# Kernel tuning notes

Hardware: AMD Instinct MI355X
Metric: run time of the kernel (lower is better)

Reference implementation:

```python
import jax, jax.numpy as jnp
import numpy as np

NUM_HEADS = 8
ROPE_BASE = 10000.0


def _rope_cache(T, D, dtype=jnp.float32):
    # LLaMA-style rope cache: cos/sin of shape [T, D]
    inv_freq = 1.0 / (ROPE_BASE ** (jnp.arange(0, D, 2, dtype=dtype) / D))
    t = jnp.arange(T, dtype=dtype)
    freqs = t[:, None] * inv_freq[None, :]            # [T, D/2]
    emb = jnp.concatenate([freqs, freqs], axis=-1)    # [T, D]
    return jnp.cos(emb), jnp.sin(emb)


def _rotate_half(x):
    x1, x2 = jnp.split(x, 2, axis=-1)
    return jnp.concatenate([-x2, x1], axis=-1)


def setup_inputs() -> dict:
    key = jax.random.key(0)
    k1, k2, k3 = jax.random.split(key, 3)
    B, T, C = 4, 2048, 512
    x = jax.random.normal(k1, (B, T, C), dtype=jnp.float32)
    Wqkv = jax.random.normal(k2, (C, 3 * C), dtype=jnp.float32) * (1.0 / np.sqrt(C))
    Wproj = jax.random.normal(k3, (C, C), dtype=jnp.float32) * (1.0 / np.sqrt(C))
    return {"x": x, "Wqkv": Wqkv, "Wproj": Wproj}


def reference(x, Wqkv, Wproj):
    B, T, C = x.shape
    H = NUM_HEADS
    D = C // H

    qkv = jnp.einsum('btc,cf->btf', x, Wqkv)          # [B,T,3C]
    qkv = qkv.reshape(B, T, H, 3 * D)
    q, k, v = jnp.split(qkv, 3, axis=-1)              # each [B,T,H,D]
    q = q.transpose(0, 2, 1, 3)                       # [B,H,T,D]
    k = k.transpose(0, 2, 1, 3)
    v = v.transpose(0, 2, 1, 3)

    cos, sin = _rope_cache(T, D, dtype=x.dtype)       # [T,D]
    cos = cos[None, None, :, :]
    sin = sin[None, None, :, :]
    q = q * cos + _rotate_half(q) * sin
    k = k * cos + _rotate_half(k) * sin

    scale = 1.0 / np.sqrt(D)
    scores = jnp.einsum('bhqd,bhkd->bhqk', q, k) * scale  # [B,H,T,T]
    causal = jnp.tril(jnp.ones((T, T), dtype=bool))
    scores = jnp.where(causal[None, None, :, :], scores, jnp.finfo(scores.dtype).min)
    attn = jax.nn.softmax(scores, axis=-1)
    out = jnp.einsum('bhqk,bhkd->bhqd', attn, v)      # [B,H,T,D]
    out = out.transpose(0, 2, 1, 3).reshape(B, T, C)
    return jnp.einsum('btc,cd->btd', out, Wproj)
```

## Files before the change

kernel.cpp:

```cpp
#include <hip/hip_runtime.h>
#include <hip/hip_bf16.h>
#include <stdint.h>

constexpr int Bn = 4;
constexpr int Tn = 2048;
constexpr int Cn = 512;
constexpr int Hn = 8;
constexpr int Dn = 64;
constexpr int BT = Bn * Tn;
constexpr int NQKV = 3 * Cn;

typedef __attribute__((ext_vector_type(4))) float  f32x4;
typedef __attribute__((ext_vector_type(8))) short  s16x8;
typedef __attribute__((ext_vector_type(4))) short  s16x4;

__device__ __forceinline__ short f2bs(float f) {
    __hip_bfloat16 h = __float2bfloat16(f);
    return *reinterpret_cast<short*>(&h);
}

__device__ __forceinline__ void gload16(const short* g, short* l) {
    __builtin_amdgcn_global_load_lds(
        (const __attribute__((address_space(1))) void*)g,
        (__attribute__((address_space(3))) void*)l, 16, 0, 0);
}


__global__ __launch_bounds__(256) void k_prep(const float* __restrict__ x,
                                              const float* __restrict__ Wqkv,
                                              const float* __restrict__ Wproj,
                                              short* __restrict__ xb,
                                              short* __restrict__ wqkvT,
                                              short* __restrict__ wprojT,
                                              float2* __restrict__ csT) {
    const int bid = blockIdx.x;
    const int tid = threadIdx.x;
    __shared__ float lds[64 * 65];

    if (bid < 4096) {
        int i = bid * 256 + tid;
        f32x4 v = reinterpret_cast<const f32x4*>(x)[i];
        s16x4 o;
        o[0] = f2bs(v[0]); o[1] = f2bs(v[1]); o[2] = f2bs(v[2]); o[3] = f2bs(v[3]);
        reinterpret_cast<s16x4*>(xb)[i] = o;
    } else if (bid < 4352) {
        int wb = bid - 4096;
        const float* W; short* out; int N, n0, k0;
        if (wb < 192) {
            W = Wqkv; out = wqkvT; N = NQKV;
            n0 = (wb >> 3) * 64; k0 = (wb & 7) * 64;
        } else {
            wb -= 192;
            W = Wproj; out = wprojT; N = Cn;
            n0 = (wb >> 3) * 64; k0 = (wb & 7) * 64;
        }
#pragma unroll
        for (int i = 0; i < 16; ++i) {
            int flat = i * 256 + tid;
            int k = flat >> 6, n = flat & 63;
            lds[n * 65 + k] = W[(size_t)(k0 + k) * N + n0 + n];
        }
        __syncthreads();
#pragma unroll
        for (int i = 0; i < 16; ++i) {
            int flat = i * 256 + tid;
            int n = flat >> 6, k = flat & 63;
            out[(size_t)(n0 + n) * 512 + k0 + k] = f2bs(lds[n * 65 + k]);
        }
    } else {
        int i = (bid - 4352) * 256 + tid;
        int t = i >> 6, d = i & 63;
        float inv = exp2f(-(float)(d & 31) * 0.41524101186f);
        float fr = (float)t * inv;
        csT[i] = make_float2(cosf(fr), sinf(fr));
    }
}


template <int MODE>
__global__ __launch_bounds__(256, 2) void gemm_kernel(
    const short* __restrict__ A, const short* __restrict__ Bt,
    const float2* __restrict__ csT,
    short* __restrict__ Qb, short* __restrict__ Kb, short* __restrict__ Vt,
    float* __restrict__ outF) {
    const int m0 = blockIdx.y * 128;
    const int n0 = blockIdx.x * 128;
    const int tid = threadIdx.x;
    const int w = tid >> 6, lane = tid & 63;
    const int qi = lane & 15, g = lane >> 4;
    const int wr = w >> 1, wc = w & 1;

    __shared__ short As[2][128 * 64];
    __shared__ short Bs[2][128 * 64];

    f32x4 acc[4][4];
#pragma unroll
    for (int mt = 0; mt < 4; ++mt)
#pragma unroll
        for (int nt = 0; nt < 4; ++nt) acc[mt][nt] = (f32x4){0.f, 0.f, 0.f, 0.f};

    const int lr = lane >> 3;
    const int lc = (lane & 7) ^ lr;

#define STAGEG(buf, k0)                                                         \
    {                                                                           \
        _Pragma("unroll")                                                       \
        for (int s4_ = 0; s4_ < 4; ++s4_) {                                     \
            int slot_ = s4_ * 4 + w;                                            \
            int r_ = slot_ * 8 + lr;                                            \
            gload16(&A[(size_t)(m0 + r_) * 512 + (k0) + lc * 8],                \
                    &As[buf][slot_ * 512 + lane * 8]);                          \
            gload16(&Bt[(size_t)(n0 + r_) * 512 + (k0) + lc * 8],               \
                    &Bs[buf][slot_ * 512 + lane * 8]);                          \
        }                                                                       \
    }

    STAGEG(0, 0);
    __syncthreads();

    for (int it = 0; it < 8; ++it) {
        if (it + 1 < 8) STAGEG((it + 1) & 1, (it + 1) * 64);
        const int cur = it & 1;
#pragma unroll
        for (int kk = 0; kk < 2; ++kk) {
            s16x8 af[4], bf[4];
#pragma unroll
            for (int mt = 0; mt < 4; ++mt) {
                int row = wr * 64 + mt * 16 + qi;
                af[mt] = *(const s16x8*)&As[cur][row * 64 + (((kk << 2) | g) ^ (qi & 7)) * 8];
            }
#pragma unroll
            for (int nt = 0; nt < 4; ++nt) {
                int row = wc * 64 + nt * 16 + qi;
                bf[nt] = *(const s16x8*)&Bs[cur][row * 64 + (((kk << 2) | g) ^ (qi & 7)) * 8];
            }
#pragma unroll
            for (int mt = 0; mt < 4; ++mt)
#pragma unroll
                for (int nt = 0; nt < 4; ++nt)
                    acc[mt][nt] = __builtin_amdgcn_mfma_f32_16x16x32_bf16(
                        af[mt], bf[nt], acc[mt][nt], 0, 0, 0);
        }
        __syncthreads();
    }
#undef STAGEG

    if (MODE == 1) {
#pragma unroll
        for (int mt = 0; mt < 4; ++mt)
#pragma unroll
            for (int nt = 0; nt < 4; ++nt)
#pragma unroll
                for (int r = 0; r < 4; ++r)
                    outF[(size_t)(m0 + wr * 64 + mt * 16 + 4 * g + r) * 512 +
                         n0 + wc * 64 + nt * 16 + qi] = acc[mt][nt][r];
    } else {
        const int seg64 = (n0 >> 6) + wc;
        const int h = seg64 / 3;
        const int seg = seg64 % 3;
        const int b = m0 >> 11;
        const int tb = (m0 & 2047) + wr * 64;
        const float QSC = 0.125f * 1.44269504f;
        if (seg == 2) {
            const size_t vbase = (size_t)(b * Hn + h) * Dn;
#pragma unroll
            for (int mt = 0; mt < 4; ++mt)
#pragma unroll
                for (int nt = 0; nt < 4; ++nt)
#pragma unroll
                    for (int r = 0; r < 4; ++r) {
                        int t = tb + mt * 16 + 4 * g + r;
                        int d = nt * 16 + qi;
                        int o = t & 31;
                        int jj = (t & ~31) + ((o >> 2) & 3) * 8 + (o >> 4) * 4 + (o & 3);
                        Vt[(vbase + d) * Tn + jj] = f2bs(acc[mt][nt][r]);
                    }
        } else {
            short* dst = (seg == 0) ? Qb : Kb;
            const float post = (seg == 0) ? QSC : 1.0f;
            const size_t headbase = (size_t)(b * Hn + h) * Tn;
#pragma unroll
            for (int mt = 0; mt < 4; ++mt)
#pragma unroll
                for (int nt = 0; nt < 4; ++nt)
#pragma unroll
                    for (int r = 0; r < 4; ++r) {
                        int t = tb + mt * 16 + 4 * g + r;
                        int d = nt * 16 + qi;
                        float val = acc[mt][nt][r];
                        float pv = (nt < 2) ? -acc[mt][nt + 2][r] : acc[mt][nt - 2][r];
                        float2 cs = csT[t * 64 + d];
                        dst[(headbase + t) * Dn + d] = f2bs((val * cs.x + pv * cs.y) * post);
                    }
        }
    }
}


__global__ __launch_bounds__(256, 4) void attn_kernel(const short* __restrict__ Qb,
                                                      const short* __restrict__ Kb,
                                                      const short* __restrict__ Vt,
                                                      short* __restrict__ AO) {
    const int idx = blockIdx.x;
    const int bh = idx & 31;
    const int qt = 31 - (idx >> 5);
    const int q0 = qt * 64;
    const int tid = threadIdx.x;
    const int w = tid >> 6, lane = tid & 63;
    const int qi = lane & 15, g = lane >> 4;
    const int b = bh >> 3, h = bh & 7;

    __shared__ short Ks[2][64 * 64];
    __shared__ short Vs[2][64 * 64];

    const short* Qh = Qb + (size_t)bh * Tn * Dn;
    const short* Kh = Kb + (size_t)bh * Tn * Dn;
    const short* Vh = Vt + (size_t)bh * Dn * Tn;

    const int wrow0 = q0 + w * 16;
    s16x8 qf[2];
#pragma unroll
    for (int dh = 0; dh < 2; ++dh)
        qf[dh] = *(const s16x8*)&Qh[(size_t)(wrow0 + qi) * Dn + dh * 32 + g * 8];

    f32x4 O[4];
#pragma unroll
    for (int dt = 0; dt < 4; ++dt) O[dt] = (f32x4){0.f, 0.f, 0.f, 0.f};
    float lsum = 0.f;

    const int nch = qt + 1;
    const f32x4 z4 = {0.f, 0.f, 0.f, 0.f};

    const int lr = lane >> 3;
    const int lc = (lane & 7) ^ lr;

#define STAGE(buf, ch)                                                          \
    {                                                                           \
        const int kv0_ = (ch) * 64;                                             \
        _Pragma("unroll")                                                       \
        for (int i_ = 0; i_ < 2; ++i_) {                                        \
            int slot_ = i_ * 4 + w;                                             \
            int r_ = slot_ * 8 + lr;                                            \
            gload16(&Kh[(size_t)(kv0_ + r_) * 64 + lc * 8],                     \
                    &Ks[buf][slot_ * 512 + lane * 8]);                          \
            gload16(&Vh[(size_t)r_ * Tn + kv0_ + lc * 8],                       \
                    &Vs[buf][slot_ * 512 + lane * 8]);                          \
        }                                                                       \
    }

    STAGE(0, 0);

    for (int ch = 0; ch < nch; ++ch) {
        const int kv0 = ch * 64;
        const int cur = ch & 1;
        if (ch + 1 < nch) {
            STAGE((ch + 1) & 1, ch + 1);
            asm volatile("s_waitcnt vmcnt(4)" ::: "memory");
        } else {
            asm volatile("s_waitcnt vmcnt(0)" ::: "memory");
        }
        __builtin_amdgcn_s_barrier();
        asm volatile("" ::: "memory");

        if (kv0 <= wrow0 + 15) {
            f32x4 sacc[4];
#pragma unroll
            for (int sub = 0; sub < 4; ++sub) {
                const int krow = sub * 16 + qi;
                s16x8 ka = *(const s16x8*)&Ks[cur][krow * 64 + ((g ^ (qi & 7))) * 8];
                s16x8 kc = *(const s16x8*)&Ks[cur][krow * 64 + (((4 | g) ^ (qi & 7))) * 8];
                f32x4 t0 = __builtin_amdgcn_mfma_f32_16x16x32_bf16(ka, qf[0], z4, 0, 0, 0);
                sacc[sub] = __builtin_amdgcn_mfma_f32_16x16x32_bf16(kc, qf[1], t0, 0, 0, 0);
            }

            float pe[16];
            if (kv0 + 63 <= wrow0) {
#pragma unroll
                for (int e2 = 0; e2 < 16; ++e2)
                    pe[e2] = exp2f(sacc[e2 >> 2][e2 & 3]);
            } else {
                const int qrow = wrow0 + qi;
#pragma unroll
                for (int sub = 0; sub < 4; ++sub)
#pragma unroll
                    for (int r = 0; r < 4; ++r) {
                        int key = kv0 + sub * 16 + 4 * g + r;
                        pe[sub * 4 + r] = (key <= qrow) ? exp2f(sacc[sub][r]) : 0.f;
                    }
            }
            {
                float a0 = (pe[0] + pe[1]) + (pe[2] + pe[3]);
                float a1 = (pe[4] + pe[5]) + (pe[6] + pe[7]);
                float a2 = (pe[8] + pe[9]) + (pe[10] + pe[11]);
                float a3 = (pe[12] + pe[13]) + (pe[14] + pe[15]);
                lsum += (a0 + a1) + (a2 + a3);
            }
            s16x8 pf[2];
#pragma unroll
            for (int c = 0; c < 2; ++c)
#pragma unroll
                for (int e2 = 0; e2 < 8; ++e2) pf[c][e2] = f2bs(pe[c * 8 + e2]);

#pragma unroll
            for (int c = 0; c < 2; ++c)
#pragma unroll
                for (int dt = 0; dt < 4; ++dt) {
                    const int vrow = dt * 16 + qi;
                    s16x8 vf = *(const s16x8*)&Vs[cur][vrow * 64 +
                                                       ((((c << 2) | g) ^ (qi & 7))) * 8];
                    O[dt] = __builtin_amdgcn_mfma_f32_16x16x32_bf16(
                        pf[c], vf, O[dt], 0, 0, 0);
                }
        }
        asm volatile("" ::: "memory");
        __builtin_amdgcn_s_barrier();
        asm volatile("" ::: "memory");
    }
#undef STAGE

    lsum += __shfl_xor(lsum, 16);
    lsum += __shfl_xor(lsum, 32);

#pragma unroll
    for (int r = 0; r < 4; ++r) {
        float li = __shfl(lsum, 4 * g + r);
        float inv = 1.f / li;
        int t = wrow0 + 4 * g + r;
#pragma unroll
        for (int dt = 0; dt < 4; ++dt)
            AO[((size_t)(b * Tn + t)) * Cn + h * 64 + dt * 16 + qi] =
                f2bs(O[dt][r] * inv);
    }
}


extern "C" void kernel_launch(void* const* d_in, const int* in_sizes, int n_in,
                              void* d_out, int out_size, void* d_ws, size_t ws_size,
                              hipStream_t stream) {
    const float* x = (const float*)d_in[0];
    const float* Wqkv = (const float*)d_in[1];
    const float* Wproj = (const float*)d_in[2];
    float* out = (float*)d_out;

    char* ws = (char*)d_ws;
    size_t o = 0;
    short* xb = (short*)(ws + o);      o += (size_t)BT * Cn * 2;
    short* wqkvT = (short*)(ws + o);   o += (size_t)NQKV * Cn * 2;
    short* wprojT = (short*)(ws + o);  o += (size_t)Cn * Cn * 2;
    short* Qb = (short*)(ws + o);      o += (size_t)Bn * Hn * Tn * Dn * 2;
    short* Kb = (short*)(ws + o);      o += (size_t)Bn * Hn * Tn * Dn * 2;
    short* Vt = (short*)(ws + o);      o += (size_t)Bn * Hn * Tn * Dn * 2;
    float2* csT = (float2*)(ws + o);   o += (size_t)Tn * Dn * 8;

    k_prep<<<dim3(4864), 256, 0, stream>>>(x, Wqkv, Wproj, xb, wqkvT, wprojT, csT);

    gemm_kernel<0><<<dim3(NQKV / 128, BT / 128), 256, 0, stream>>>(
        xb, wqkvT, csT, Qb, Kb, Vt, nullptr);

    attn_kernel<<<dim3(1024), 256, 0, stream>>>(Qb, Kb, Vt, xb );

    gemm_kernel<1><<<dim3(Cn / 128, BT / 128), 256, 0, stream>>>(
        xb , wprojT, csT, nullptr, nullptr, nullptr, out);
}
```

Before: 89.74 us.

## Split attention KV range across two wave groups and merge partial outputs

Doubles the attention block to 512 threads, with two groups of four waves each processing half of the causal KV chunks for the same 64 query rows. Each group gets its own double-buffered K/V shared memory. The partial O and row sums are combined through shared memory before normalization and store. This is meant to shorten the serial KV loop per block, which matters most for the long causal rows. It also adds s_setprio around the MFMA sections. The costs are double the LDS per block, an extra reduction and barriers, and possibly lower occupancy.

```diff
diff --git a/kernel.cpp b/kernel.cpp
--- a/kernel.cpp
+++ b/kernel.cpp
@@ -197,7 +197,7 @@
 }
 
 
-__global__ __launch_bounds__(256, 4) void attn_kernel(const short* __restrict__ Qb,
+__global__ __launch_bounds__(512, 4) void attn_kernel(const short* __restrict__ Qb,
                                                       const short* __restrict__ Kb,
                                                       const short* __restrict__ Vt,
                                                       short* __restrict__ AO) {
@@ -208,16 +208,18 @@
     const int tid = threadIdx.x;
     const int w = tid >> 6, lane = tid & 63;
     const int qi = lane & 15, g = lane >> 4;
+    const int grp = w >> 2;
+    const int wg = w & 3;
     const int b = bh >> 3, h = bh & 7;
 
-    __shared__ short Ks[2][64 * 64];
-    __shared__ short Vs[2][64 * 64];
+    __shared__ short Ks[2][2][64 * 64];
+    __shared__ short Vs[2][2][64 * 64];
 
     const short* Qh = Qb + (size_t)bh * Tn * Dn;
     const short* Kh = Kb + (size_t)bh * Tn * Dn;
     const short* Vh = Vt + (size_t)bh * Dn * Tn;
 
-    const int wrow0 = q0 + w * 16;
+    const int wrow0 = q0 + wg * 16;
     s16x8 qf[2];
 #pragma unroll
     for (int dh = 0; dh < 2; ++dh)
@@ -229,6 +231,9 @@
     float lsum = 0.f;
 
     const int nch = qt + 1;
+    const int mid = (nch + 1) >> 1;
+    const int chbase = grp ? mid : 0;
+    const int nmy = grp ? (nch - mid) : mid;
     const f32x4 z4 = {0.f, 0.f, 0.f, 0.f};
 
     const int lr = lane >> 3;
@@ -239,39 +244,45 @@
         const int kv0_ = (ch) * 64;                                             \
         _Pragma("unroll")                                                       \
         for (int i_ = 0; i_ < 2; ++i_) {                                        \
-            int slot_ = i_ * 4 + w;                                             \
+            int slot_ = i_ * 4 + wg;                                            \
             int r_ = slot_ * 8 + lr;                                            \
             gload16(&Kh[(size_t)(kv0_ + r_) * 64 + lc * 8],                     \
-                    &Ks[buf][slot_ * 512 + lane * 8]);                          \
+                    &Ks[grp][buf][slot_ * 512 + lane * 8]);                     \
             gload16(&Vh[(size_t)r_ * Tn + kv0_ + lc * 8],                       \
-                    &Vs[buf][slot_ * 512 + lane * 8]);                          \
+                    &Vs[grp][buf][slot_ * 512 + lane * 8]);                     \
         }                                                                       \
     }
 
-    STAGE(0, 0);
-
-    for (int ch = 0; ch < nch; ++ch) {
+    if (nmy > 0) STAGE(0, chbase);
+
+    for (int i = 0; i < mid; ++i) {
+        const bool valid = i < nmy;
+        const int ch = chbase + i;
         const int kv0 = ch * 64;
-        const int cur = ch & 1;
-        if (ch + 1 < nch) {
-            STAGE((ch + 1) & 1, ch + 1);
-            asm volatile("s_waitcnt vmcnt(4)" ::: "memory");
-        } else {
-            asm volatile("s_waitcnt vmcnt(0)" ::: "memory");
+        const int cur = i & 1;
+        if (valid) {
+            if (i + 1 < nmy) {
+                STAGE((i + 1) & 1, ch + 1);
+                asm volatile("s_waitcnt vmcnt(4)" ::: "memory");
+            } else {
+                asm volatile("s_waitcnt vmcnt(0)" ::: "memory");
+            }
         }
         __builtin_amdgcn_s_barrier();
         asm volatile("" ::: "memory");
 
-        if (kv0 <= wrow0 + 15) {
+        if (valid) {
             f32x4 sacc[4];
+            __builtin_amdgcn_s_setprio(1);
 #pragma unroll
             for (int sub = 0; sub < 4; ++sub) {
                 const int krow = sub * 16 + qi;
-                s16x8 ka = *(const s16x8*)&Ks[cur][krow * 64 + ((g ^ (qi & 7))) * 8];
-                s16x8 kc = *(const s16x8*)&Ks[cur][krow * 64 + (((4 | g) ^ (qi & 7))) * 8];
+                s16x8 ka = *(const s16x8*)&Ks[grp][cur][krow * 64 + ((g ^ (qi & 7))) * 8];
+                s16x8 kc = *(const s16x8*)&Ks[grp][cur][krow * 64 + (((4 | g) ^ (qi & 7))) * 8];
                 f32x4 t0 = __builtin_amdgcn_mfma_f32_16x16x32_bf16(ka, qf[0], z4, 0, 0, 0);
                 sacc[sub] = __builtin_amdgcn_mfma_f32_16x16x32_bf16(kc, qf[1], t0, 0, 0, 0);
             }
+            __builtin_amdgcn_s_setprio(0);
 
             float pe[16];
             if (kv0 + 63 <= wrow0) {
@@ -301,16 +312,18 @@
 #pragma unroll
                 for (int e2 = 0; e2 < 8; ++e2) pf[c][e2] = f2bs(pe[c * 8 + e2]);
 
+            __builtin_amdgcn_s_setprio(1);
 #pragma unroll
             for (int c = 0; c < 2; ++c)
 #pragma unroll
                 for (int dt = 0; dt < 4; ++dt) {
                     const int vrow = dt * 16 + qi;
-                    s16x8 vf = *(const s16x8*)&Vs[cur][vrow * 64 +
-                                                       ((((c << 2) | g) ^ (qi & 7))) * 8];
+                    s16x8 vf = *(const s16x8*)&Vs[grp][cur][vrow * 64 +
+                                                   ((((c << 2) | g) ^ (qi & 7))) * 8];
                     O[dt] = __builtin_amdgcn_mfma_f32_16x16x32_bf16(
                         pf[c], vf, O[dt], 0, 0, 0);
                 }
+            __builtin_amdgcn_s_setprio(0);
         }
         asm volatile("" ::: "memory");
         __builtin_amdgcn_s_barrier();
@@ -321,15 +334,33 @@
     lsum += __shfl_xor(lsum, 16);
     lsum += __shfl_xor(lsum, 32);
 
-#pragma unroll
-    for (int r = 0; r < 4; ++r) {
-        float li = __shfl(lsum, 4 * g + r);
-        float inv = 1.f / li;
-        int t = wrow0 + 4 * g + r;
+    f32x4* Osc = (f32x4*)&Ks[0][0][0];
+    float* Lsc = (float*)&Vs[0][0][0];
+    __syncthreads();
+    if (grp == 1) {
 #pragma unroll
         for (int dt = 0; dt < 4; ++dt)
-            AO[((size_t)(b * Tn + t)) * Cn + h * 64 + dt * 16 + qi] =
-                f2bs(O[dt][r] * inv);
+            Osc[(dt * 4 + wg) * 64 + lane] = O[dt];
+        if (g == 0) Lsc[wg * 16 + qi] = lsum;
+    }
+    __syncthreads();
+    if (grp == 0) {
+        float lt = lsum + Lsc[wg * 16 + qi];
+#pragma unroll
+        for (int dt = 0; dt < 4; ++dt) {
+            f32x4 p = Osc[(dt * 4 + wg) * 64 + lane];
+            O[dt][0] += p[0]; O[dt][1] += p[1]; O[dt][2] += p[2]; O[dt][3] += p[3];
+        }
+#pragma unroll
+        for (int r = 0; r < 4; ++r) {
+            float li = __shfl(lt, 4 * g + r);
+            float inv = 1.f / li;
+            int t = wrow0 + 4 * g + r;
+#pragma unroll
+            for (int dt = 0; dt < 4; ++dt)
+                AO[((size_t)(b * Tn + t)) * Cn + h * 64 + dt * 16 + qi] =
+                    f2bs(O[dt][r] * inv);
+        }
     }
 }
 
@@ -357,7 +388,7 @@
     gemm_kernel<0><<<dim3(NQKV / 128, BT / 128), 256, 0, stream>>>(
         xb, wqkvT, csT, Qb, Kb, Vt, nullptr);
 
-    attn_kernel<<<dim3(1024), 256, 0, stream>>>(Qb, Kb, Vt, xb );
+    attn_kernel<<<dim3(1024), 512, 0, stream>>>(Qb, Kb, Vt, xb );
 
     gemm_kernel<1><<<dim3(Cn / 128, BT / 128), 256, 0, stream>>>(
         xb , wprojT, csT, nullptr, nullptr, nullptr, out);
```

New measurement: 87.23 us. 1.03x faster.
